# Kernel optimization log

Measured on AMD Instinct MI355X. Metric: run time of the kernel, lower is better.

The kernel has to match this reference:

```python
import jax, jax.numpy as jnp
import numpy as np
from jax import lax

NYQ = 11025.0
N_SAMPLES = 2 ** 15
N_FRAMES = 128
N_HARM = 16
FILT = 64
N_NOTES = 128
MIN_F0 = 40.0 / NYQ
MAX_F0 = 3000.0 / NYQ
F0_SPAN = MAX_F0 - MIN_F0
MIN_RES = 0.1
RES_SPAN = 1.0 - MIN_RES
# musical scale center frequencies (chromatic, A4=440) normalized by nyquist
FREQS = jnp.asarray((440.0 * 2.0 ** ((np.arange(N_NOTES) - 69) / 12.0)) / NYQ, dtype=jnp.float32)
HARM_FACTORS = jnp.arange(1, N_HARM + 1, dtype=jnp.float32)


def lerp1d(x, out_size):
    # torch F.interpolate(mode='linear', align_corners=False) on last axis
    L = x.shape[-1]
    scale = L / out_size
    coords = (jnp.arange(out_size, dtype=jnp.float32) + 0.5) * scale - 0.5
    coords = jnp.clip(coords, 0.0, L - 1)
    i0 = jnp.floor(coords).astype(jnp.int32)
    i1 = jnp.minimum(i0 + 1, L - 1)
    w = (coords - i0).astype(x.dtype)
    return x[..., i0] * (1.0 - w) + x[..., i1] * w


def setup_inputs() -> dict:
    key = jax.random.key(0)
    k1, k2, k3 = jax.random.split(key, 3)
    batch = 64
    packed = jax.random.uniform(k1, (batch, 480), dtype=jnp.float32)
    gumbel_u = jax.random.uniform(k2, (batch, N_NOTES), dtype=jnp.float32)
    noise_u = jax.random.uniform(k3, (batch, 1, N_SAMPLES), dtype=jnp.float32)
    return {"packed": packed, "gumbel_u": gumbel_u, "noise_u": noise_u}


def _forward(packed, gumbel_u, noise_u):
    B = packed.shape[0]
    # param slices
    f0_logits = packed[:, 0:128]
    amp = packed[:, 256:384].reshape(B, 1, N_FRAMES) * 2.0 - 1.0
    harm_amp = packed[:, 384:400]                      # (B, 16)
    harm_decay = MIN_RES + packed[:, 400:416] * RES_SPAN  # (B, 16)
    noise_filter = packed[:, 416:480].reshape(B, 1, FILT)

    # hard gumbel-softmax f0 selection (straight-through)
    eps = 1e-10
    g = -jnp.log(-jnp.log(gumbel_u + eps) + eps)
    y_soft = jax.nn.softmax(f0_logits + g, axis=-1)
    y_hard = jax.nn.one_hot(jnp.argmax(y_soft, axis=-1), N_NOTES, dtype=y_soft.dtype)
    y = lax.stop_gradient(y_hard - y_soft) + y_soft
    f0 = (y @ FREQS)[:, None, None] * jnp.ones((1, 1, N_FRAMES), jnp.float32)  # (B,1,128)
    f0 = f0 * NYQ
    f0 = MIN_F0 + f0 * F0_SPAN
    # (note: f0_fine is computed but discarded in the original module)

    # harmonic oscillator bank
    osc = f0 * HARM_FACTORS[None, :, None]            # (B,16,128)
    radians = osc / NYQ * jnp.float32(np.pi)
    radians = lerp1d(radians, N_SAMPLES)              # (B,16,32768)
    osc_bank = jnp.sin(jnp.cumsum(radians, axis=-1))

    amp_full = lerp1d(amp, N_SAMPLES)                 # (B,1,32768)

    # FFT-filtered noise
    nf = lerp1d(noise_filter, N_SAMPLES // 2)
    nf = jnp.pad(nf, ((0, 0), (0, 0), (0, 1)))        # (B,1,16385)
    noise = noise_u * 2.0 - 1.0
    spec = jnp.fft.rfft(noise, axis=-1, norm='ortho')
    noise = jnp.fft.irfft(spec * nf, n=N_SAMPLES, axis=-1, norm='ortho')
    noise = noise * jnp.clip(amp_full, 0.0, 1.0)

    # per-frame decay recurrence (scan over 128 frames)
    def step(cur, a_i):  # cur (B,16), a_i (B,)
        cur = jnp.clip(cur + a_i[:, None] * harm_amp, 0.0, 1.0)
        return cur * harm_decay, cur

    _, env = lax.scan(step, jnp.zeros((B, N_HARM), jnp.float32), amp[:, 0, :].T)
    env = jnp.transpose(env, (1, 2, 0))               # (B,16,128)
    env_full = lerp1d(env, N_SAMPLES)

    x = env_full * osc_bank
    x = noise + x
    return jnp.mean(x, axis=(0, 1), keepdims=True)    # (1,1,32768)


def reference(packed, gumbel_u, noise_u):
    return _forward(packed, gumbel_u, noise_u)
```

## Files before the change

### kernel.cpp

```cpp
#include <hip/hip_runtime.h>
#include <math.h>

#define NSAMP   32768
#define NFRAMES 128
#define NHARM   16
#define BATCH   64
#define MFFT    16384
#define ZROW    137

static __device__ __forceinline__ float clampf(float x, float lo, float hi) {
  return fminf(fmaxf(x, lo), hi);
}
static __device__ __forceinline__ int zp(int fft, int p) {
  return fft * ZROW + p + (p >> 4);
}
static __device__ __forceinline__ int brev7(int n) {
  return (int)(__brev((unsigned)n) >> 25);
}
static __device__ __forceinline__ float2 cmulf(float c, float s, float2 v) {
  return make_float2(c * v.x - s * v.y, c * v.y + s * v.x);
}
static __device__ __forceinline__ float2 f2add(float2 a, float2 b) {
  return make_float2(a.x + b.x, a.y + b.y);
}
static __device__ __forceinline__ float2 f2sub(float2 a, float2 b) {
  return make_float2(a.x - b.x, a.y - b.y);
}

static __device__ __forceinline__ void tw_init(float2* tws, int tid) {
  if (tid < 64) {
    float s, c;
    __sincosf(-(float)M_PI * (float)tid * (1.0f / 64.0f), &s, &c);
    tws[tid] = make_float2(c, s);
  }
}

template <int NT, bool INV>
static __device__ __forceinline__ void fft128_r4(float2* zs, const float2* tws, int tid) {
  constexpr int NF = NT / 32;
  int fft = tid >> 5, i = tid & 31;
  #pragma unroll
  for (int s = 0; s < 6; s += 2) {
    int half = 1 << s;
    int kk1 = i & (half - 1);
    int base = ((i & ~(half - 1)) << 2) | kk1;
    int p0 = zp(fft, base),            p1 = zp(fft, base + half);
    int p2 = zp(fft, base + 2 * half), p3 = zp(fft, base + 3 * half);
    float2 q0 = zs[p0], q1 = zs[p1], q2 = zs[p2], q3 = zs[p3];
    float2 t1 = tws[kk1 << (6 - s)], t2 = tws[kk1 << (5 - s)];
    float c1 = t1.x, s1 = INV ? -t1.y : t1.y;
    float c2 = t2.x, s2 = INV ? -t2.y : t2.y;
    float c2b = INV ? -s2 : s2, s2b = INV ? c2 : -c2;
    float2 t;
    t = cmulf(c1, s1, q1);   float2 A0 = f2add(q0, t), A1 = f2sub(q0, t);
    t = cmulf(c1, s1, q3);   float2 A2 = f2add(q2, t), A3 = f2sub(q2, t);
    t = cmulf(c2, s2, A2);   zs[p0] = f2add(A0, t); zs[p2] = f2sub(A0, t);
    t = cmulf(c2b, s2b, A3); zs[p1] = f2add(A1, t); zs[p3] = f2sub(A1, t);
    __syncthreads();
  }
  #pragma unroll
  for (int j = tid; j < NF * 64; j += NT) {
    int f = j >> 6, kk = j & 63;
    float2 w = tws[kk];
    float cc = w.x, ss = INV ? -w.y : w.y;
    int a0 = zp(f, kk), a1 = zp(f, kk + 64);
    float2 a = zs[a0], bv = zs[a1];
    float2 t = cmulf(cc, ss, bv);
    zs[a0] = f2add(a, t); zs[a1] = f2sub(a, t);
  }
  __syncthreads();
}

template <int NT>
static __device__ __forceinline__ void fft128_r4_dif_inv(float2* zs, const float2* tws, int tid) {
  constexpr int NF = NT / 32;
  #pragma unroll
  for (int j = tid; j < NF * 64; j += NT) {
    int f = j >> 6, kk = j & 63;
    float2 w = tws[kk];
    float cc = w.x, ss = -w.y;
    int a0 = zp(f, kk), a1 = zp(f, kk + 64);
    float2 u = zs[a0], v = zs[a1];
    zs[a0] = f2add(u, v);
    zs[a1] = cmulf(cc, ss, f2sub(u, v));
  }
  __syncthreads();
  int fft = tid >> 5, i = tid & 31;
  #pragma unroll
  for (int s = 4; s >= 0; s -= 2) {
    int half = 1 << s;
    int kk1 = i & (half - 1);
    int base = ((i & ~(half - 1)) << 2) | kk1;
    int p0 = zp(fft, base),            p1 = zp(fft, base + half);
    int p2 = zp(fft, base + 2 * half), p3 = zp(fft, base + 3 * half);
    float2 q0 = zs[p0], q1 = zs[p1], q2 = zs[p2], q3 = zs[p3];
    float2 t1 = tws[kk1 << (6 - s)], t2 = tws[kk1 << (5 - s)];
    float c1 = t1.x, s1 = -t1.y;
    float c2 = t2.x, s2 = -t2.y;
    float c2b = -s2, s2b = c2;
    float2 B0 = f2add(q0, q2);
    float2 B2 = cmulf(c2, s2, f2sub(q0, q2));
    float2 B1 = f2add(q1, q3);
    float2 B3 = cmulf(c2b, s2b, f2sub(q1, q3));
    zs[p0] = f2add(B0, B1);
    zs[p1] = cmulf(c1, s1, f2sub(B0, B1));
    zs[p2] = f2add(B2, B3);
    zs[p3] = cmulf(c1, s1, f2sub(B2, B3));
    __syncthreads();
  }
}

static __device__ __forceinline__ float h_filter(int f, const float* nf_s) {
  float coords = ((float)f + 0.5f) * (1.0f / 256.0f) - 0.5f;
  coords = clampf(coords, 0.0f, 63.0f);
  int i0 = (int)coords;
  int i1 = (i0 < 63) ? (i0 + 1) : 63;
  float w = coords - (float)i0;
  return nf_s[i0] * (1.0f - w) + nf_s[i1] * w;
}

static __device__ __forceinline__ float amp_lerp(int s, const float* amp_s) {
  float coords = ((float)s + 0.5f) * (1.0f / 256.0f) - 0.5f;
  coords = clampf(coords, 0.0f, 127.0f);
  int i0 = (int)coords;
  int i1 = (i0 < 127) ? (i0 + 1) : 127;
  float w = coords - (float)i0;
  float v = amp_s[i0] * (1.0f - w) + amp_s[i1] * w;
  return clampf(v, 0.0f, 1.0f);
}

static __device__ void k1_body(
    const float* __restrict__ packed, const float* __restrict__ gumbel,
    double* __restrict__ r64_ws, float* __restrict__ env_ws, int b, int tid) {
  __shared__ double zv[128];
  __shared__ int    zi[128];
  __shared__ double f0_sh;
  const float* pk = packed + b * 480;

  double u = (double)gumbel[b * 128 + tid];
  double t = -log(u + 1e-10);
  double g = -log(t + 1e-10);
  zv[tid] = (double)pk[tid] + g;
  zi[tid] = tid;
  __syncthreads();
  for (int s = 64; s > 0; s >>= 1) {
    if (tid < s) {
      double a = zv[tid], c = zv[tid + s];
      int ia = zi[tid], ic = zi[tid + s];
      if (c > a || (c == a && ic < ia)) { zv[tid] = c; zi[tid] = ic; }
    }
    __syncthreads();
  }
  if (tid == 0) {
    int note = zi[0];
    double Fd  = 440.0 * exp2(((double)(note - 69)) / 12.0) / 11025.0;
    float  F32 = (float)Fd;
    double f0  = (double)F32 * 11025.0;
    f0 = (40.0 / 11025.0) + f0 * (3000.0 / 11025.0 - 40.0 / 11025.0);
    f0_sh = f0;
  }
  __syncthreads();
  if (tid < NHARM) {
    int h = tid;
    int c = b * NHARM + h;
    const float PIF = 3.14159265358979323846f;
    double osc = f0_sh * (double)(h + 1);
    r64_ws[c] = (osc / 11025.0) * (double)PIF;
    float ha = pk[384 + h];
    float hd = 0.1f + pk[400 + h] * 0.9f;
    float cur = 0.0f;
    for (int tt = 0; tt < NFRAMES; ++tt) {
      float a = pk[256 + tt] * 2.0f - 1.0f;
      cur = clampf(cur + a * ha, 0.0f, 1.0f);
      env_ws[tt * 1024 + c] = cur;
      cur = cur * hd;
    }
  }
}

__global__ __launch_bounds__(128, 4) void kf1(
    const float* __restrict__ noise_u, float2* __restrict__ A,
    const float* __restrict__ packed, const float* __restrict__ gumbel,
    double* __restrict__ r64_ws, float* __restrict__ env_ws) {
  int b = blockIdx.x, tid = threadIdx.x;
  if (blockIdx.y == 0) { k1_body(packed, gumbel, r64_ws, env_ws, b, tid); return; }
  int tile = blockIdx.y - 1;
  __shared__ float2 zs[4 * ZROW];
  __shared__ float2 tws[64];
  tw_init(tws, tid);
  const float2* nu2 = (const float2*)(noise_u + (size_t)b * NSAMP);
  #pragma unroll
  for (int it = 0; it < 4; ++it) {
    int e = it * 128 + tid;
    int n1 = e >> 2, n2l = e & 3;
    float2 xv = nu2[n1 * 128 + tile * 4 + n2l];
    zs[zp(n2l, brev7(n1))] = make_float2(xv.x * 2.0f - 1.0f, xv.y * 2.0f - 1.0f);
  }
  __syncthreads();
  fft128_r4<128, false>(zs, tws, tid);
  float2* Ab = A + (size_t)b * MFFT;
  #pragma unroll
  for (int it = 0; it < 4; ++it) {
    int e = it * 128 + tid;
    int k1 = e >> 2, n2l = e & 3;
    int n2 = tile * 4 + n2l;
    float2 v = zs[zp(n2l, k1)];
    float ang = -(2.0f * (float)M_PI / 16384.0f) * (float)(k1 * n2);
    float ss, cc; __sincosf(ang, &ss, &cc);
    Ab[k1 * 128 + n2] = make_float2(cc * v.x - ss * v.y, cc * v.y + ss * v.x);
  }
}

__global__ __launch_bounds__(128, 4) void kmid(
    const float* __restrict__ packed, float2* __restrict__ A) {
  __shared__ float2 zs[4 * ZROW];
  __shared__ float2 tws[64];
  __shared__ float  nf_s[64];
  __shared__ int    rowk1[4];
  int b = blockIdx.x, t = blockIdx.y, tid = threadIdx.x;
  tw_init(tws, tid);
  if (tid >= 64 && tid < 128) nf_s[tid - 64] = packed[b * 480 + 416 + (tid - 64)];
  if (tid < 4) {
    int s = tid & 1;
    int m = t * 2 + s;
    rowk1[tid] = (tid < 2) ? m : ((m == 0) ? 64 : 128 - m);
  }
  __syncthreads();
  float2* Ab = A + (size_t)b * MFFT;

  #pragma unroll
  for (int it = 0; it < 4; ++it) {
    int e = it * 128 + tid;
    int r = e >> 7, n2 = e & 127;
    zs[zp(r, brev7(n2))] = Ab[rowk1[r] * 128 + n2];
  }
  __syncthreads();
  fft128_r4<128, false>(zs, tws, tid);

  const float hsc = 1.0f / 16384.0f;
  #pragma unroll
  for (int it = 0; it < 2; ++it) {
    int task = it * 128 + tid;
    int r  = task >> 6;
    int k2 = task & 63;
    int k1 = rowk1[r];
    int f = k1 + (k2 << 7);
    if (f == 0) {
      float2 Z0 = zs[zp(0, 0)];
      float X0 = Z0.x + Z0.y;
      float Y0 = X0 * (h_filter(0, nf_s) * hsc);
      zs[zp(0, 0)] = make_float2(0.5f * Y0, 0.5f * Y0);
      float Hm = h_filter(8192, nf_s) * hsc;
      float2 Zm = zs[zp(0, 64)];
      zs[zp(0, 64)] = make_float2(Zm.x * Hm, Zm.y * Hm);
    } else {
      int g = 16384 - f;
      int k1g = g & 127;
      int pr = (k1g == k1) ? r : ((r < 2) ? r + 2 : r - 2);
      int k2p = g >> 7;
      float2 Zf = zs[zp(r, k2)], Zg = zs[zp(pr, k2p)];
      float Ax = 0.5f * (Zf.x + Zg.x), Ay = 0.5f * (Zf.y - Zg.y);
      float Bx = 0.5f * (Zf.x - Zg.x), By = 0.5f * (Zf.y + Zg.y);
      float ang = (-(float)M_PI / (float)MFFT) * (float)f;
      float ss, cc; __sincosf(ang, &ss, &cc);
      float WBx = cc * Bx - ss * By, WBy = cc * By + ss * Bx;
      float Hf = h_filter(f, nf_s) * hsc;
      float Hg = h_filter(g, nf_s) * hsc;
      float Yfx = (Ax + WBy) * Hf, Yfy = (Ay - WBx) * Hf;
      float Ygx = (Ax - WBy) * Hg, Ygy = (-Ay - WBx) * Hg;
      float A2x = 0.5f * (Yfx + Ygx), A2y = 0.5f * (Yfy - Ygy);
      float B2x = 0.5f * (Yfx - Ygx), B2y = 0.5f * (Yfy + Ygy);
      float CBx = cc * B2x + ss * B2y;
      float CBy = cc * B2y - ss * B2x;
      zs[zp(r, k2)]   = make_float2(A2x - CBy, A2y + CBx);
      float DBx = cc * B2x + ss * B2y;
      float DBy = ss * B2x - cc * B2y;
      zs[zp(pr, k2p)] = make_float2(A2x - DBy, -A2y + DBx);
    }
  }
  __syncthreads();

  fft128_r4_dif_inv<128>(zs, tws, tid);

  #pragma unroll
  for (int it = 0; it < 4; ++it) {
    int e = it * 128 + tid;
    int r = e >> 7, n2 = e & 127;
    int k1 = rowk1[r];
    float2 v = zs[zp(r, brev7(n2))];
    float ang = (2.0f * (float)M_PI / 16384.0f) * (float)(k1 * n2);
    float ss, cc; __sincosf(ang, &ss, &cc);
    Ab[k1 * 128 + n2] = make_float2(cc * v.x - ss * v.y, cc * v.y + ss * v.x);
  }
}

__global__ __launch_bounds__(128, 4) void ki2(
    const float* __restrict__ packed, const float2* __restrict__ A,
    float2* __restrict__ ws2) {
  __shared__ float2 zs[4 * ZROW];
  __shared__ float2 tws[64];
  __shared__ float amp_s[128];
  int b = blockIdx.x, tile = blockIdx.y, tid = threadIdx.x;
  tw_init(tws, tid);
  amp_s[tid] = packed[b * 480 + 256 + tid] * 2.0f - 1.0f;
  const float2* Ab = A + (size_t)b * MFFT;
  #pragma unroll
  for (int it = 0; it < 4; ++it) {
    int e = it * 128 + tid;
    int k1 = e >> 2, n2l = e & 3;
    zs[zp(n2l, brev7(k1))] = Ab[k1 * 128 + tile * 4 + n2l];
  }
  __syncthreads();
  fft128_r4<128, true>(zs, tws, tid);
  float2* W2 = ws2 + (size_t)b * MFFT;
  #pragma unroll
  for (int it = 0; it < 4; ++it) {
    int e = it * 128 + tid;
    int n1 = e >> 2, n2l = e & 3;
    int n2 = tile * 4 + n2l;
    int n = n1 * 128 + n2;
    float2 v = zs[zp(n2l, n1)];
    v.x *= amp_lerp(2 * n,     amp_s);
    v.y *= amp_lerp(2 * n + 1, amp_s);
    W2[n] = v;
  }
}

__global__ __launch_bounds__(1024) void k3r(
    const double* __restrict__ r64_ws, const float* __restrict__ env_ws,
    const float* __restrict__ ws2f, float* __restrict__ out) {
  __shared__ float oscs[128];
  __shared__ float nse[8][128];
  const double TWO_PI     = 6.283185307179586476925286766559;
  const double INV_TWO_PI = 0.15915494309189533576888376337251;
  int tid = threadIdx.x;
  int lane = tid & 63;
  int wv = tid >> 6;
  int k = blockIdx.x;
  int s0 = k * 128;
  int K = k >> 1, half = k & 1;

  double r0 = r64_ws[lane * 16];
  double rr = r0 - rint(r0 * INV_TWO_PI) * TWO_PI;
  double x0 = (double)(s0 + wv * 8 + 1) * r0;
  double ph = x0 - rint(x0 * INV_TWO_PI) * TWO_PI;
  float s1, c1, srot, crot;
  __sincosf((float)ph, &s1, &c1);
  __sincosf((float)rr, &srot, &crot);

  int km1 = (K > 0) ? (K - 1) : 0;
  int kp1 = (K < 127) ? (K + 1) : 127;
  int fA = half ? K : km1;
  int fB = half ? kp1 : K;
  const float4* eA = (const float4*)(env_ws + fA * 1024 + lane * 16);
  const float4* eB = (const float4*)(env_ws + fB * 1024 + lane * 16);
  float ev[16], sl[16];
  float basew = (half ? 0.5f : 128.5f) + (float)(wv * 8);
  #pragma unroll
  for (int q = 0; q < 4; ++q) {
    float4 a = eA[q], bb = eB[q];
    float d;
    d = (bb.x - a.x) * (1.0f / 256.0f); sl[q*4+0] = d; ev[q*4+0] = a.x + d * basew;
    d = (bb.y - a.y) * (1.0f / 256.0f); sl[q*4+1] = d; ev[q*4+1] = a.y + d * basew;
    d = (bb.z - a.z) * (1.0f / 256.0f); sl[q*4+2] = d; ev[q*4+2] = a.z + d * basew;
    d = (bb.w - a.w) * (1.0f / 256.0f); sl[q*4+3] = d; ev[q*4+3] = a.w + d * basew;
  }

  #pragma unroll
  for (int j = 0; j < 8; ++j) {
    float twoC = c1 + c1;
    float sm1 = 0.0f, sc = s1;
    float acc = ev[0] * sc; ev[0] += sl[0];
    #pragma unroll
    for (int i = 1; i < 16; ++i) {
      float sn = fmaf(twoC, sc, -sm1);
      sm1 = sc; sc = sn;
      acc = fmaf(ev[i], sn, acc);
      ev[i] += sl[i];
    }
    acc += __shfl_xor(acc, 32);
    acc += __shfl_xor(acc, 16);
    acc += __shfl_xor(acc, 8);
    acc += __shfl_xor(acc, 4);
    acc += __shfl_xor(acc, 2);
    acc += __shfl_xor(acc, 1);
    if (lane == 0) oscs[wv * 8 + j] = acc;
    float tn = fmaf(s1, crot, c1 * srot);
    c1 = fmaf(c1, crot, -(s1 * srot));
    s1 = tn;
  }
  __syncthreads();

  {
    int j = tid & 127, grp = tid >> 7;
    const float* src = ws2f + (size_t)(grp * 8) * NSAMP + s0 + j;
    float acc = 0.0f;
    #pragma unroll
    for (int bb = 0; bb < 8; ++bb) acc += src[(size_t)bb * NSAMP];
    nse[grp][j] = acc;
  }
  __syncthreads();

  if (tid < 128) {
    float nz = 0.0f;
    #pragma unroll
    for (int g = 0; g < 8; ++g) nz += nse[g][tid];
    out[s0 + tid] = oscs[tid] * (1.0f / 1024.0f) + nz * (1.0f / 64.0f);
  }
}

extern "C" void kernel_launch(void* const* d_in, const int* in_sizes, int n_in,
                              void* d_out, int out_size, void* d_ws, size_t ws_size,
                              hipStream_t stream) {
  const float* packed  = (const float*)d_in[0];
  const float* gumbel  = (const float*)d_in[1];
  const float* noise_u = (const float*)d_in[2];
  float* out = (float*)d_out;

  char* wsc = (char*)d_ws;
  double* r64_ws = (double*)wsc;
  float*  env_ws = (float*)(wsc + 8192);
  float2* A      = (float2*)(wsc + 8192 + 524288);
  float2* ws2    = (float2*)(wsc + 8192 + 524288 + (size_t)BATCH * MFFT * 8);

  kf1 <<<dim3(BATCH, 33), 128, 0, stream>>>(noise_u, A, packed, gumbel, r64_ws, env_ws);
  kmid<<<dim3(BATCH, 32), 128, 0, stream>>>(packed, A);
  ki2 <<<dim3(BATCH, 32), 128, 0, stream>>>(packed, A, ws2);
  k3r <<<256, 1024, 0, stream>>>(r64_ws, env_ws, (const float*)ws2, out);
}
```

Before: 37.69 us.

## Fold oscillator synthesis into kmid and accumulate noise into output with atomics

Removes the final k3r kernel. The harmonic oscillator sum is now computed at the tail of each kmid block, with 2048 blocks each writing 16 output samples. The noise inverse-FFT stage in ki2 atomically adds its scaled batch contribution directly into the output. This drops one kernel launch and the 8 MB ws2 intermediate write and read-back, at the cost of 64-way float atomic contention per output sample and non-deterministic summation order. It also relies on kmid's plain store finishing before ki2's atomics, which stream ordering provides.

```diff
diff --git a/kernel.cpp b/kernel.cpp
--- a/kernel.cpp
+++ b/kernel.cpp
@@ -35,9 +35,8 @@
   }
 }
 
-template <int NT, bool INV>
+template <bool INV>
 static __device__ __forceinline__ void fft128_r4(float2* zs, const float2* tws, int tid) {
-  constexpr int NF = NT / 32;
   int fft = tid >> 5, i = tid & 31;
   #pragma unroll
   for (int s = 0; s < 6; s += 2) {
@@ -59,7 +58,7 @@
     __syncthreads();
   }
   #pragma unroll
-  for (int j = tid; j < NF * 64; j += NT) {
+  for (int j = tid; j < 256; j += 128) {
     int f = j >> 6, kk = j & 63;
     float2 w = tws[kk];
     float cc = w.x, ss = INV ? -w.y : w.y;
@@ -71,11 +70,9 @@
   __syncthreads();
 }
 
-template <int NT>
 static __device__ __forceinline__ void fft128_r4_dif_inv(float2* zs, const float2* tws, int tid) {
-  constexpr int NF = NT / 32;
-  #pragma unroll
-  for (int j = tid; j < NF * 64; j += NT) {
+  #pragma unroll
+  for (int j = tid; j < 256; j += 128) {
     int f = j >> 6, kk = j & 63;
     float2 w = tws[kk];
     float cc = w.x, ss = -w.y;
@@ -197,7 +194,7 @@
     zs[zp(n2l, brev7(n1))] = make_float2(xv.x * 2.0f - 1.0f, xv.y * 2.0f - 1.0f);
   }
   __syncthreads();
-  fft128_r4<128, false>(zs, tws, tid);
+  fft128_r4<false>(zs, tws, tid);
   float2* Ab = A + (size_t)b * MFFT;
   #pragma unroll
   for (int it = 0; it < 4; ++it) {
@@ -212,7 +209,9 @@
 }
 
 __global__ __launch_bounds__(128, 4) void kmid(
-    const float* __restrict__ packed, float2* __restrict__ A) {
+    const float* __restrict__ packed, float2* __restrict__ A,
+    const double* __restrict__ r64_ws, const float* __restrict__ env_ws,
+    float* __restrict__ out) {
   __shared__ float2 zs[4 * ZROW];
   __shared__ float2 tws[64];
   __shared__ float  nf_s[64];
@@ -235,7 +234,7 @@
     zs[zp(r, brev7(n2))] = Ab[rowk1[r] * 128 + n2];
   }
   __syncthreads();
-  fft128_r4<128, false>(zs, tws, tid);
+  fft128_r4<false>(zs, tws, tid);
 
   const float hsc = 1.0f / 16384.0f;
   #pragma unroll
@@ -280,7 +279,7 @@
   }
   __syncthreads();
 
-  fft128_r4_dif_inv<128>(zs, tws, tid);
+  fft128_r4_dif_inv(zs, tws, tid);
 
   #pragma unroll
   for (int it = 0; it < 4; ++it) {
@@ -292,11 +291,75 @@
     float ss, cc; __sincosf(ang, &ss, &cc);
     Ab[k1 * 128 + n2] = make_float2(cc * v.x - ss * v.y, cc * v.y + ss * v.x);
   }
+
+  {
+    __shared__ float oscs[16];
+    const double TWO_PI     = 6.283185307179586476925286766559;
+    const double INV_TWO_PI = 0.15915494309189533576888376337251;
+    int gid = b * 32 + t;
+    int lane = tid & 63;
+    int w = tid >> 6;
+    int chunk = gid >> 3, sub = gid & 7;
+    int s0 = chunk * 128 + sub * 16;
+    int K = chunk >> 1, half = chunk & 1;
+
+    double r0 = r64_ws[lane * 16];
+    double rr = r0 - rint(r0 * INV_TWO_PI) * TWO_PI;
+    double x0 = (double)(s0 + w * 8 + 1) * r0;
+    double ph = x0 - rint(x0 * INV_TWO_PI) * TWO_PI;
+    float s1, c1, srot, crot;
+    __sincosf((float)ph, &s1, &c1);
+    __sincosf((float)rr, &srot, &crot);
+
+    int km1 = (K > 0) ? (K - 1) : 0;
+    int kp1 = (K < 127) ? (K + 1) : 127;
+    int fA = half ? K : km1;
+    int fB = half ? kp1 : K;
+    const float4* eA = (const float4*)(env_ws + fA * 1024 + lane * 16);
+    const float4* eB = (const float4*)(env_ws + fB * 1024 + lane * 16);
+    float ev[16], sl[16];
+    float basew = (half ? 0.5f : 128.5f) + (float)(sub * 16 + w * 8);
+    #pragma unroll
+    for (int q = 0; q < 4; ++q) {
+      float4 a = eA[q], bb = eB[q];
+      float d;
+      d = (bb.x - a.x) * (1.0f / 256.0f); sl[q*4+0] = d; ev[q*4+0] = a.x + d * basew;
+      d = (bb.y - a.y) * (1.0f / 256.0f); sl[q*4+1] = d; ev[q*4+1] = a.y + d * basew;
+      d = (bb.z - a.z) * (1.0f / 256.0f); sl[q*4+2] = d; ev[q*4+2] = a.z + d * basew;
+      d = (bb.w - a.w) * (1.0f / 256.0f); sl[q*4+3] = d; ev[q*4+3] = a.w + d * basew;
+    }
+
+    #pragma unroll
+    for (int j = 0; j < 8; ++j) {
+      float twoC = c1 + c1;
+      float sm1 = 0.0f, sc = s1;
+      float acc = ev[0] * sc; ev[0] += sl[0];
+      #pragma unroll
+      for (int i = 1; i < 16; ++i) {
+        float sn = fmaf(twoC, sc, -sm1);
+        sm1 = sc; sc = sn;
+        acc = fmaf(ev[i], sn, acc);
+        ev[i] += sl[i];
+      }
+      acc += __shfl_xor(acc, 32);
+      acc += __shfl_xor(acc, 16);
+      acc += __shfl_xor(acc, 8);
+      acc += __shfl_xor(acc, 4);
+      acc += __shfl_xor(acc, 2);
+      acc += __shfl_xor(acc, 1);
+      if (lane == 0) oscs[w * 8 + j] = acc;
+      float tn = fmaf(s1, crot, c1 * srot);
+      c1 = fmaf(c1, crot, -(s1 * srot));
+      s1 = tn;
+    }
+    __syncthreads();
+    if (tid < 16) out[s0 + tid] = oscs[tid] * (1.0f / 1024.0f);
+  }
 }
 
 __global__ __launch_bounds__(128, 4) void ki2(
     const float* __restrict__ packed, const float2* __restrict__ A,
-    float2* __restrict__ ws2) {
+    float* __restrict__ out) {
   __shared__ float2 zs[4 * ZROW];
   __shared__ float2 tws[64];
   __shared__ float amp_s[128];
@@ -311,8 +374,7 @@
     zs[zp(n2l, brev7(k1))] = Ab[k1 * 128 + tile * 4 + n2l];
   }
   __syncthreads();
-  fft128_r4<128, true>(zs, tws, tid);
-  float2* W2 = ws2 + (size_t)b * MFFT;
+  fft128_r4<true>(zs, tws, tid);
   #pragma unroll
   for (int it = 0; it < 4; ++it) {
     int e = it * 128 + tid;
@@ -320,92 +382,8 @@
     int n2 = tile * 4 + n2l;
     int n = n1 * 128 + n2;
     float2 v = zs[zp(n2l, n1)];
-    v.x *= amp_lerp(2 * n,     amp_s);
-    v.y *= amp_lerp(2 * n + 1, amp_s);
-    W2[n] = v;
-  }
-}
-
-__global__ __launch_bounds__(1024) void k3r(
-    const double* __restrict__ r64_ws, const float* __restrict__ env_ws,
-    const float* __restrict__ ws2f, float* __restrict__ out) {
-  __shared__ float oscs[128];
-  __shared__ float nse[8][128];
-  const double TWO_PI     = 6.283185307179586476925286766559;
-  const double INV_TWO_PI = 0.15915494309189533576888376337251;
-  int tid = threadIdx.x;
-  int lane = tid & 63;
-  int wv = tid >> 6;
-  int k = blockIdx.x;
-  int s0 = k * 128;
-  int K = k >> 1, half = k & 1;
-
-  double r0 = r64_ws[lane * 16];
-  double rr = r0 - rint(r0 * INV_TWO_PI) * TWO_PI;
-  double x0 = (double)(s0 + wv * 8 + 1) * r0;
-  double ph = x0 - rint(x0 * INV_TWO_PI) * TWO_PI;
-  float s1, c1, srot, crot;
-  __sincosf((float)ph, &s1, &c1);
-  __sincosf((float)rr, &srot, &crot);
-
-  int km1 = (K > 0) ? (K - 1) : 0;
-  int kp1 = (K < 127) ? (K + 1) : 127;
-  int fA = half ? K : km1;
-  int fB = half ? kp1 : K;
-  const float4* eA = (const float4*)(env_ws + fA * 1024 + lane * 16);
-  const float4* eB = (const float4*)(env_ws + fB * 1024 + lane * 16);
-  float ev[16], sl[16];
-  float basew = (half ? 0.5f : 128.5f) + (float)(wv * 8);
-  #pragma unroll
-  for (int q = 0; q < 4; ++q) {
-    float4 a = eA[q], bb = eB[q];
-    float d;
-    d = (bb.x - a.x) * (1.0f / 256.0f); sl[q*4+0] = d; ev[q*4+0] = a.x + d * basew;
-    d = (bb.y - a.y) * (1.0f / 256.0f); sl[q*4+1] = d; ev[q*4+1] = a.y + d * basew;
-    d = (bb.z - a.z) * (1.0f / 256.0f); sl[q*4+2] = d; ev[q*4+2] = a.z + d * basew;
-    d = (bb.w - a.w) * (1.0f / 256.0f); sl[q*4+3] = d; ev[q*4+3] = a.w + d * basew;
-  }
-
-  #pragma unroll
-  for (int j = 0; j < 8; ++j) {
-    float twoC = c1 + c1;
-    float sm1 = 0.0f, sc = s1;
-    float acc = ev[0] * sc; ev[0] += sl[0];
-    #pragma unroll
-    for (int i = 1; i < 16; ++i) {
-      float sn = fmaf(twoC, sc, -sm1);
-      sm1 = sc; sc = sn;
-      acc = fmaf(ev[i], sn, acc);
-      ev[i] += sl[i];
-    }
-    acc += __shfl_xor(acc, 32);
-    acc += __shfl_xor(acc, 16);
-    acc += __shfl_xor(acc, 8);
-    acc += __shfl_xor(acc, 4);
-    acc += __shfl_xor(acc, 2);
-    acc += __shfl_xor(acc, 1);
-    if (lane == 0) oscs[wv * 8 + j] = acc;
-    float tn = fmaf(s1, crot, c1 * srot);
-    c1 = fmaf(c1, crot, -(s1 * srot));
-    s1 = tn;
-  }
-  __syncthreads();
-
-  {
-    int j = tid & 127, grp = tid >> 7;
-    const float* src = ws2f + (size_t)(grp * 8) * NSAMP + s0 + j;
-    float acc = 0.0f;
-    #pragma unroll
-    for (int bb = 0; bb < 8; ++bb) acc += src[(size_t)bb * NSAMP];
-    nse[grp][j] = acc;
-  }
-  __syncthreads();
-
-  if (tid < 128) {
-    float nz = 0.0f;
-    #pragma unroll
-    for (int g = 0; g < 8; ++g) nz += nse[g][tid];
-    out[s0 + tid] = oscs[tid] * (1.0f / 1024.0f) + nz * (1.0f / 64.0f);
+    atomicAdd(&out[2 * n],     v.x * amp_lerp(2 * n,     amp_s) * (1.0f / 64.0f));
+    atomicAdd(&out[2 * n + 1], v.y * amp_lerp(2 * n + 1, amp_s) * (1.0f / 64.0f));
   }
 }
 
@@ -421,10 +399,8 @@
   double* r64_ws = (double*)wsc;
   float*  env_ws = (float*)(wsc + 8192);
   float2* A      = (float2*)(wsc + 8192 + 524288);
-  float2* ws2    = (float2*)(wsc + 8192 + 524288 + (size_t)BATCH * MFFT * 8);
 
   kf1 <<<dim3(BATCH, 33), 128, 0, stream>>>(noise_u, A, packed, gumbel, r64_ws, env_ws);
-  kmid<<<dim3(BATCH, 32), 128, 0, stream>>>(packed, A);
-  ki2 <<<dim3(BATCH, 32), 128, 0, stream>>>(packed, A, ws2);
-  k3r <<<256, 1024, 0, stream>>>(r64_ws, env_ws, (const float*)ws2, out);
-}
+  kmid<<<dim3(BATCH, 32), 128, 0, stream>>>(packed, A, r64_ws, env_ws, out);
+  ki2 <<<dim3(BATCH, 32), 128, 0, stream>>>(packed, A, out);
+}
```

Measured after the change: 66.57 us. 76.7% more time.
